# Performance work log

Hardware: AMD Instinct MI355X
Metric: run time of the kernel (lower is better)

The kernel has to match this reference:

```python
import jax, jax.numpy as jnp
import numpy as np


def _conv(x, w, pad, groups=1):
    # NCHW conv, stride 1
    return jax.lax.conv_general_dilated(
        x, w, (1, 1), [(pad, pad), (pad, pad)],
        feature_group_count=groups,
        dimension_numbers=('NCHW', 'OIHW', 'NCHW'))


def _ss2d(x, in_proj_w, conv_w, conv_b, xproj_w, dtproj_w, dtproj_b,
          A_logs, Ds, ln_g, ln_b, out_proj_w):
    # x: (B, C, H, W); VMamba-style SS2D with K=4 directional scans.
    Bb, C, H, W = x.shape
    D = conv_w.shape[0]          # d_inner = 2 * d_model
    N = A_logs.shape[-1]         # d_state
    R = dtproj_w.shape[-1]       # dt_rank
    L = H * W

    # in_proj (no bias), split into x and gate z
    xz = jnp.einsum('bchw,ec->behw', x, in_proj_w)      # (B, 2D, H, W)
    xin, z = jnp.split(xz, 2, axis=1)
    # depthwise conv + SiLU
    xc = jax.nn.silu(_conv(xin, conv_w, 1, groups=D) + conv_b[None, :, None, None])

    # build 4 scan orders: row-major, col-major, and their reverses
    xf = xc.reshape(Bb, D, L)
    xt = xc.transpose(0, 1, 3, 2).reshape(Bb, D, L)
    xs = jnp.stack([xf, xt, xf[..., ::-1], xt[..., ::-1]], axis=1)  # (B, 4, D, L)

    x_dbl = jnp.einsum('bkdl,kcd->bkcl', xs, xproj_w)   # (B, 4, R+2N, L)
    dt, Bmat, Cmat = jnp.split(x_dbl, [R, R + N], axis=2)
    delta = jax.nn.softplus(
        jnp.einsum('bkrl,kdr->bkdl', dt, dtproj_w) + dtproj_b[None, :, :, None])
    A = -jnp.exp(A_logs)                                 # (4, D, N)

    def step(h, t):
        u_t, d_t, b_t, c_t = t                           # (B,4,D),(B,4,D),(B,4,N),(B,4,N)
        h = jnp.exp(d_t[..., None] * A) * h + (d_t * u_t)[..., None] * b_t[:, :, None, :]
        return h, jnp.einsum('bkdn,bkn->bkd', h, c_t)

    tm = lambda a: jnp.moveaxis(a, -1, 0)                # time-major
    h0 = jnp.zeros((Bb, 4, D, N), x.dtype)
    _, ys = jax.lax.scan(step, h0, (tm(xs), tm(delta), tm(Bmat), tm(Cmat)))
    out_y = jnp.moveaxis(ys, 0, -1) + Ds[None, :, :, None] * xs    # (B, 4, D, L)

    inv_y = out_y[:, 2:4, :, ::-1]
    unT = lambda a: a.reshape(Bb, D, W, H).transpose(0, 1, 3, 2).reshape(Bb, D, L)
    y = out_y[:, 0] + inv_y[:, 0] + unT(out_y[:, 1]) + unT(inv_y[:, 1])  # (B, D, L)

    y = y.reshape(Bb, D, H, W).transpose(0, 2, 3, 1)     # (B, H, W, D)
    mu = y.mean(-1, keepdims=True)
    var = y.var(-1, keepdims=True)
    y = (y - mu) / jnp.sqrt(var + 1e-5) * ln_g + ln_b    # out_norm (LayerNorm)
    y = y * jax.nn.silu(z.transpose(0, 2, 3, 1))         # gate
    out = jnp.einsum('bhwd,cd->bhwc', y, out_proj_w)     # out_proj (no bias)
    return out.transpose(0, 3, 1, 2)                     # back to NCHW


def _forward(x, fc1_w, bn1_s, bn1_b, dw3_w, dw3_b, pw1_w, pw1_b,
             dw5_w, dw5_b, pw2_w, pw2_b, fc2_w, bn2_s, bn2_b,
             in_proj_w, conv_w, conv_b, xproj_w, dtproj_w, dtproj_b,
             A_logs, Ds, ln_g, ln_b, out_proj_w):
    relu6 = lambda v: jnp.clip(v, 0.0, 6.0)
    Cc = x.shape[1]
    # fc1: 1x1 conv + folded BN + ReLU6
    h = relu6(_conv(x, fc1_w, 0) * bn1_s[None, :, None, None] + bn1_b[None, :, None, None])
    Ch = h.shape[1]
    # depthwise(3) + pointwise
    x1 = _conv(_conv(h, dw3_w, 1, groups=Ch) + dw3_b[None, :, None, None], pw1_w, 0) \
         + pw1_b[None, :, None, None]
    # depthwise(5) + pointwise
    x2 = _conv(_conv(h, dw5_w, 2, groups=Ch) + dw5_b[None, :, None, None], pw2_w, 0) \
         + pw2_b[None, :, None, None]
    # SS2D attention branch
    x3 = _ss2d(h, in_proj_w, conv_w, conv_b, xproj_w, dtproj_w, dtproj_b,
               A_logs, Ds, ln_g, ln_b, out_proj_w)
    # fc2: 1x1 conv + folded BN, then ReLU6
    out = relu6(_conv(x1 + x2 + x3, fc2_w, 0) * bn2_s[None, :, None, None]
                + bn2_b[None, :, None, None])
    return out


def setup_inputs() -> dict:
    key = jax.random.key(0)
    ks = jax.random.split(key, 24)
    B, C, H, W = 4, 96, 64, 64
    D, N, R, K = 192, 16, 6, 4   # d_inner=2*96, d_state, dt_rank=ceil(96/16), 4 scans
    rn = lambda k, s, sc: jax.random.normal(k, s, jnp.float32) * sc
    return {
        'x': rn(ks[0], (B, C, H, W), 1.0),
        'fc1_w': rn(ks[1], (C, C, 1, 1), 0.1),
        'bn1_s': 1.0 + rn(ks[2], (C,), 0.05),
        'bn1_b': rn(ks[3], (C,), 0.05),
        'dw3_w': rn(ks[4], (C, 1, 3, 3), 0.2),
        'dw3_b': rn(ks[5], (C,), 0.02),
        'pw1_w': rn(ks[6], (C, C, 1, 1), 0.1),
        'pw1_b': rn(ks[7], (C,), 0.02),
        'dw5_w': rn(ks[8], (C, 1, 5, 5), 0.1),
        'dw5_b': rn(ks[9], (C,), 0.02),
        'pw2_w': rn(ks[10], (C, C, 1, 1), 0.1),
        'pw2_b': rn(ks[11], (C,), 0.02),
        'fc2_w': rn(ks[12], (C, C, 1, 1), 0.1),
        'bn2_s': 1.0 + rn(ks[13], (C,), 0.05),
        'bn2_b': rn(ks[14], (C,), 0.05),
        'in_proj_w': rn(ks[15], (2 * D, C), 0.05),
        'conv_w': rn(ks[16], (D, 1, 3, 3), 0.2),
        'conv_b': rn(ks[17], (D,), 0.02),
        'xproj_w': rn(ks[18], (K, R + 2 * N, D), 0.05),
        'dtproj_w': rn(ks[19], (K, D, R), 0.1),
        'dtproj_b': jnp.full((K, D), float(np.log(np.expm1(0.01))), jnp.float32)
                    + rn(ks[20], (K, D), 0.1),
        'A_logs': jnp.broadcast_to(
            jnp.log(jnp.arange(1, N + 1, dtype=jnp.float32)), (K, D, N)) + 0.0,
        'Ds': jnp.ones((K, D), jnp.float32),
        'ln_g': jnp.ones((D,), jnp.float32),
        'ln_b': jnp.zeros((D,), jnp.float32),
        'out_proj_w': rn(ks[21], (C, D), 0.05),
    }


def reference(x, fc1_w, bn1_s, bn1_b, dw3_w, dw3_b, pw1_w, pw1_b,
              dw5_w, dw5_b, pw2_w, pw2_b, fc2_w, bn2_s, bn2_b,
              in_proj_w, conv_w, conv_b, xproj_w, dtproj_w, dtproj_b,
              A_logs, Ds, ln_g, ln_b, out_proj_w):
    return _forward(x, fc1_w, bn1_s, bn1_b, dw3_w, dw3_b, pw1_w, pw1_b,
                    dw5_w, dw5_b, pw2_w, pw2_b, fc2_w, bn2_s, bn2_b,
                    in_proj_w, conv_w, conv_b, xproj_w, dtproj_w, dtproj_b,
                    A_logs, Ds, ln_g, ln_b, out_proj_w)
```

## Files before the change

### kernel.cpp

```cpp
#include <hip/hip_runtime.h>
#include <hip/hip_bf16.h>

typedef __hip_bfloat16 bf16;

#define HW 4096
#define LOG2E 1.44269504088896f
#define NSEG 128
#define SEGLEN 32
#define XROW 40

__device__ __forceinline__ float silu_f(float x){ return x / (1.f + exp2f(-x*LOG2E)); }
__device__ __forceinline__ float relu6_f(float v){ return v < 0.f ? 0.f : (v > 6.f ? 6.f : v); }

#define PW_STORE 0
#define PW_ACC 1
#define PW_RELU6_F32 2
#define PW_RELU6_OUT 3
#define PW_STORE_T 4

struct PtrTab { const void* p[25]; int off[26]; };

__global__ __launch_bounds__(256) void convert_kernel(PtrTab tab, const unsigned int* araw, float* dst, int total){
  int isb = (*araw != 0u);
  for (int i = blockIdx.x*256 + threadIdx.x; i < total; i += gridDim.x*256){
    int s = 0;
    while (s < 24 && i >= tab.off[s+1]) s++;
    int j = i - tab.off[s];
    dst[i] = isb ? __bfloat162float(((const bf16*)tab.p[s])[j])
                 : ((const float*)tab.p[s])[j];
  }
}

template<int CIN>
__global__ __launch_bounds__(256) void pw_kernel(
    const float* __restrict__ in, const float* __restrict__ inT,
    const void* __restrict__ rawin,
    const float* __restrict__ w,
    const float* __restrict__ sc, const float* __restrict__ bi,
    float* __restrict__ outf, void* __restrict__ outv, const unsigned int* __restrict__ flagp,
    int CS, int ci0, int wstride, int Cout, int mode, int xsmode, int kchunks)
{
  __shared__ float in_s[CIN*64];
  __shared__ float w_s[CIN*34];
  int t = threadIdx.x;
  int gb = blockIdx.x * 64;
  int b = gb >> 12;
  int l0 = gb & 4095;
  if (xsmode) w += (size_t)(b & 3) * Cout * wstride;
  int coc = blockIdx.y * 32;
  int lg = t & 15, cg = t >> 4;

  float a00=0.f,a01=0.f,a10=0.f,a11=0.f,a20=0.f,a21=0.f,a30=0.f,a31=0.f;

  for (int kc = 0; kc < kchunks; kc++){
    int cbase = ci0 + kc*CIN;
    if (xsmode){
      int k = b & 3, breal = b >> 2;
      const float* src = (k & 1) ? inT : in;
      int rev = (k >= 2);
      for (int e = t; e < CIN*64; e += 256){
        int ci = e >> 6, j = e & 63;
        int pos = rev ? (4095 - (l0 + j)) : (l0 + j);
        in_s[e] = src[(size_t)(breal*192 + cbase + ci)*HW + pos];
      }
    } else if (rawin){
      int isb = (*flagp != 0u);
      for (int e = t; e < CIN*64; e += 256){
        int ci = e >> 6, j = e & 63;
        size_t idx = (size_t)(b*CS + cbase + ci)*HW + l0 + j;
        in_s[e] = isb ? __bfloat162float(((const bf16*)rawin)[idx])
                      : ((const float*)rawin)[idx];
      }
    } else {
      for (int e = t; e < CIN*64; e += 256){
        int ci = e >> 6, j = e & 63;
        in_s[e] = in[(size_t)(b*CS + cbase + ci)*HW + l0 + j];
      }
    }
    for (int e = t; e < CIN*32; e += 256){
      int cc = e / CIN, ci = e - cc*CIN;
      int co = coc + cc;
      w_s[ci*34 + cc] = (co < Cout) ? w[(size_t)co*wstride + cbase + ci] : 0.f;
    }
    __syncthreads();

    for (int ci = 0; ci < CIN; ci++){
      float4 iv = *(const float4*)(in_s + ci*64 + 4*lg);
      float2 wv = *(const float2*)(w_s + ci*34 + 2*cg);
      a00 += iv.x*wv.x; a01 += iv.x*wv.y;
      a10 += iv.y*wv.x; a11 += iv.y*wv.y;
      a20 += iv.z*wv.x; a21 += iv.z*wv.y;
      a30 += iv.w*wv.x; a31 += iv.w*wv.y;
    }
    if (kc + 1 < kchunks) __syncthreads();
  }

  float accv[4][2] = {{a00,a01},{a10,a11},{a20,a21},{a30,a31}};
  for (int jj = 0; jj < 2; jj++){
    int co = coc + 2*cg + jj;
    if (co >= Cout) continue;
    float add = bi ? bi[co] : 0.f;
    if (mode == PW_STORE_T){
      int pos = (co < 6) ? co : co + 2;
      for (int i=0;i<4;i++){
        size_t a = ((size_t)b*HW + l0 + 4*lg + i)*XROW + pos;
        outf[a] = accv[i][jj] + add;
      }
      continue;
    }
    size_t base = (size_t)(b*Cout + co)*HW + l0 + 4*lg;
    if (mode == PW_STORE){
      for (int i=0;i<4;i++) outf[base+i] = accv[i][jj] + add;
    } else if (mode == PW_ACC){
      for (int i=0;i<4;i++) outf[base+i] += accv[i][jj] + add;
    } else if (mode == PW_RELU6_F32){
      float s = sc[co];
      for (int i=0;i<4;i++) outf[base+i] = relu6_f(accv[i][jj]*s + add);
    } else {
      float s = sc[co];
      int isb = (*flagp != 0u);
      for (int i=0;i<4;i++){
        float v = relu6_f(accv[i][jj]*s + add);
        if (isb) ((bf16*)outv)[base+i] = __float2bfloat16(v);
        else     ((float*)outv)[base+i] = v;
      }
    }
  }
}

__global__ __launch_bounds__(256) void pwdual_kernel(
    const float* __restrict__ inA, const float* __restrict__ wA, const float* __restrict__ biA,
    const float* __restrict__ inB, const float* __restrict__ wB, const float* __restrict__ biB,
    float* __restrict__ outf)
{
  __shared__ float in_s[96*64];
  __shared__ float w_s[96*34];
  int t = threadIdx.x;
  int gb = blockIdx.x * 64;
  int b = gb >> 12;
  int l0 = gb & 4095;
  int coc = blockIdx.y * 32;
  int lg = t & 15, cg = t >> 4;

  float a00=0.f,a01=0.f,a10=0.f,a11=0.f,a20=0.f,a21=0.f,a30=0.f,a31=0.f;

  for (int kc = 0; kc < 2; kc++){
    const float* in = kc ? inB : inA;
    const float* w  = kc ? wB  : wA;
    for (int e = t; e < 96*64; e += 256){
      int ci = e >> 6, j = e & 63;
      in_s[e] = in[(size_t)(b*96 + ci)*HW + l0 + j];
    }
    for (int e = t; e < 96*32; e += 256){
      int cc = e / 96, ci = e - cc*96;
      w_s[ci*34 + cc] = w[(size_t)(coc+cc)*96 + ci];
    }
    __syncthreads();
    for (int ci = 0; ci < 96; ci++){
      float4 iv = *(const float4*)(in_s + ci*64 + 4*lg);
      float2 wv = *(const float2*)(w_s + ci*34 + 2*cg);
      a00 += iv.x*wv.x; a01 += iv.x*wv.y;
      a10 += iv.y*wv.x; a11 += iv.y*wv.y;
      a20 += iv.z*wv.x; a21 += iv.z*wv.y;
      a30 += iv.w*wv.x; a31 += iv.w*wv.y;
    }
    if (kc == 0) __syncthreads();
  }

  float accv[4][2] = {{a00,a01},{a10,a11},{a20,a21},{a30,a31}};
  for (int jj = 0; jj < 2; jj++){
    int co = coc + 2*cg + jj;
    float add = biA[co] + biB[co];
    size_t base = (size_t)(b*96 + co)*HW + l0 + 4*lg;
    for (int i=0;i<4;i++) outf[base+i] = accv[i][jj] + add;
  }
}

__global__ __launch_bounds__(256) void dwb_kernel(
  const float* __restrict__ h, const float* __restrict__ w3, const float* __restrict__ b3,
  const float* __restrict__ w5, const float* __restrict__ b5,
  float* __restrict__ t3, float* __restrict__ t5)
{
  __shared__ float halo[68*68];
  int ch = blockIdx.x;
  int c = ch % 96;
  const float* src = h + (size_t)ch*HW;
  size_t off = (size_t)ch*HW;
  int t = threadIdx.x;

  for (int e = t; e < 68*68; e += 256){
    int rr = e / 68, cc = e - rr*68;
    int y = rr - 2, x = cc - 2;
    halo[e] = (y >= 0 && y < 64 && x >= 0 && x < 64) ? src[y*64 + x] : 0.f;
  }
  float wv3[9], wv5[25];
  for (int i=0;i<9;i++)  wv3[i] = w3[c*9 + i];
  for (int i=0;i<25;i++) wv5[i] = w5[c*25 + i];
  float bias3 = b3[c], bias5 = b5[c];
  __syncthreads();

  int x = t & 63, r0 = t >> 6;
  for (int s = 0; s < 16; s++){
    int y = s*4 + r0;
    float a5 = bias5;
    #pragma unroll
    for (int dy=0; dy<5; dy++)
      #pragma unroll
      for (int dx=0; dx<5; dx++)
        a5 += halo[(y+dy)*68 + (x+dx)] * wv5[dy*5+dx];
    float a3 = bias3;
    #pragma unroll
    for (int dy=0; dy<3; dy++)
      #pragma unroll
      for (int dx=0; dx<3; dx++)
        a3 += halo[(y+1+dy)*68 + (x+1+dx)] * wv3[dy*3+dx];
    t3[off + y*64 + x] = a3;
    t5[off + y*64 + x] = a5;
  }
}

__global__ __launch_bounds__(256) void dwct_kernel(
  const float* __restrict__ xz, const float* __restrict__ w, const float* __restrict__ bi,
  float* __restrict__ xc, float* __restrict__ xcT)
{
  __shared__ float halo[66*66];
  __shared__ float tileT[64*65];
  int ch = blockIdx.x;
  int b = ch / 192, c = ch % 192;
  const float* src = xz + ((size_t)(b*384) + c)*HW;
  size_t off = (size_t)ch*HW;
  int t = threadIdx.x;

  for (int e = t; e < 66*66; e += 256){
    int rr = e / 66, cc = e - rr*66;
    int y = rr - 1, x = cc - 1;
    halo[e] = (y >= 0 && y < 64 && x >= 0 && x < 64) ? src[y*64 + x] : 0.f;
  }
  float wv[9];
  for (int i=0;i<9;i++) wv[i] = w[c*9 + i];
  float bias = bi[c];
  __syncthreads();

  int c2 = t & 63, r0 = t >> 6;
  for (int s = 0; s < 16; s++){
    int r = s*4 + r0;
    float acc = bias;
    #pragma unroll
    for (int dy=0; dy<3; dy++)
      #pragma unroll
      for (int dx=0; dx<3; dx++)
        acc += halo[(r+dy)*66 + (c2+dx)] * wv[dy*3+dx];
    acc = silu_f(acc);
    xc[off + r*64 + c2] = acc;
    tileT[c2*65 + r] = acc;
  }
  __syncthreads();
  for (int s = 0; s < 16; s++){
    int r = s*4 + r0;
    xcT[off + r*64 + c2] = tileT[r*65 + c2];
  }
}

__global__ __launch_bounds__(256) void transpose_kernel(const float* __restrict__ src, const float* __restrict__ src2, float* __restrict__ dst)
{
  __shared__ float tile[64*65];
  int ch = blockIdx.x;
  size_t off = (size_t)ch*HW;
  int c = threadIdx.x & 63, r0 = threadIdx.x >> 6;
  for (int s = 0; s < 16; s++){
    int r = s*4 + r0;
    float v = src[off + r*64 + c];
    if (src2) v += src2[off + r*64 + c];
    tile[c*65 + r] = v;
  }
  __syncthreads();
  for (int s = 0; s < 16; s++){
    int r = s*4 + r0;
    dst[off + r*64 + c] = tile[r*65 + c];
  }
}

template<int PASS>
__global__ __launch_bounds__(192) void scan_kernel(
  const float* __restrict__ xc, const float* __restrict__ xcT,
  const float* __restrict__ xdblT,
  const float* __restrict__ dtw, const float* __restrict__ dtb,
  const float* __restrict__ Ds,
  float* __restrict__ Pbuf, float* __restrict__ qbuf,
  const float* __restrict__ hinit,
  float* __restrict__ oy0, float* __restrict__ oy1T,
  float* __restrict__ oy2, float* __restrict__ oy3T)
{
  __shared__ float u_s[192*17];
  __shared__ float y_s[(PASS==2) ? 16*193 : 1];

  int d = threadIdx.x;
  int s = blockIdx.x, k = blockIdx.y, b = blockIdx.z;
  int bk = b*4 + k;
  const float* usrc = (k & 1) ? xcT : xc;
  int rev = (k >= 2);

  float w6[7];
  for (int r=0;r<6;r++) w6[r] = dtw[(size_t)(k*192+d)*6 + r];
  w6[6] = dtb[k*192 + d];
  float Dv = Ds[k*192 + d];

  float st[16];
  float sdv = 0.f;
  size_t pqbase = ((size_t)(bk*NSEG + s)*192 + d)*16;
  if (PASS==1){
    for (int n=0;n<16;n++) st[n]=0.f;
  } else {
    const float4* hp = (const float4*)(hinit + pqbase);
    float4 h0=hp[0], h1=hp[1], h2=hp[2], h3=hp[3];
    st[0]=h0.x; st[1]=h0.y; st[2]=h0.z; st[3]=h0.w;
    st[4]=h1.x; st[5]=h1.y; st[6]=h1.z; st[7]=h1.w;
    st[8]=h2.x; st[9]=h2.y; st[10]=h2.z; st[11]=h2.w;
    st[12]=h3.x; st[13]=h3.y; st[14]=h3.z; st[15]=h3.w;
  }

  const float* rowbase = xdblT + (size_t)bk*HW*XROW;

  for (int c = 0; c < SEGLEN/16; c++){
    int l0c = s*SEGLEN + c*16;
    for (int e = d; e < 192*16; e += 192){
      int j = e & 15, d2 = e >> 4;
      int pos = rev ? (4095 - (l0c + j)) : (l0c + j);
      u_s[d2*17+j] = usrc[((size_t)(b*192 + d2))*HW + pos];
    }
    __syncthreads();

    const float* rp = rowbase + (size_t)l0c*XROW;
    #pragma unroll
    for (int j=0;j<16;j++){
      float4 dt03 = *(const float4*)(rp);
      float2 dt45 = *(const float2*)(rp + 4);
      float v = w6[6] + dt03.x*w6[0] + dt03.y*w6[1] + dt03.z*w6[2] + dt03.w*w6[3]
                      + dt45.x*w6[4] + dt45.y*w6[5];
      float t = exp2f(v*LOG2E);
      float rr = 1.f/(1.f + t);
      float dv = (v > 20.f) ? v : log2f(1.f + t)*(1.f/LOG2E);
      float uv = u_s[d*17+j];
      float du = dv*uv;
      float4 B0 = *(const float4*)(rp + 8);
      float4 B1 = *(const float4*)(rp + 12);
      float4 B2 = *(const float4*)(rp + 16);
      float4 B3 = *(const float4*)(rp + 20);
      float Bv[16] = {B0.x,B0.y,B0.z,B0.w, B1.x,B1.y,B1.z,B1.w,
                      B2.x,B2.y,B2.z,B2.w, B3.x,B3.y,B3.z,B3.w};
      float a = rr;
      if (PASS==1){
        sdv += dv;
        #pragma unroll
        for (int n=0;n<16;n++){
          st[n] = a*st[n] + du*Bv[n];
          a *= rr;
        }
      } else {
        float4 C0 = *(const float4*)(rp + 24);
        float4 C1 = *(const float4*)(rp + 28);
        float4 C2 = *(const float4*)(rp + 32);
        float4 C3 = *(const float4*)(rp + 36);
        float Cv[16] = {C0.x,C0.y,C0.z,C0.w, C1.x,C1.y,C1.z,C1.w,
                        C2.x,C2.y,C2.z,C2.w, C3.x,C3.y,C3.z,C3.w};
        float y = Dv*uv;
        #pragma unroll
        for (int n=0;n<16;n++){
          st[n] = a*st[n] + du*Bv[n];
          y += st[n]*Cv[n];
          a *= rr;
        }
        y_s[j*193 + d] = y;
      }
      rp += XROW;
    }
    __syncthreads();
    if (PASS==2){
      float* dst = (k==0) ? oy0 : (k==1) ? oy1T : (k==2) ? oy2 : oy3T;
      for (int e = d; e < 16*192; e += 192){
        int j = e & 15, d2 = e >> 4;
        int pos = rev ? (4095 - (l0c + j)) : (l0c + j);
        dst[((size_t)(b*192 + d2))*HW + pos] = y_s[j*193 + d2];
      }
    }
  }

  if (PASS==1){
    float rT = exp2f(-sdv*LOG2E);
    float Pv[16];
    float pw = rT;
    for (int n=0;n<16;n++){ Pv[n]=pw; pw*=rT; }
    float4* Pp = (float4*)(Pbuf + pqbase);
    float4* qp = (float4*)(qbuf + pqbase);
    for (int i=0;i<4;i++){
      Pp[i] = make_float4(Pv[4*i], Pv[4*i+1], Pv[4*i+2], Pv[4*i+3]);
      qp[i] = make_float4(st[4*i], st[4*i+1], st[4*i+2], st[4*i+3]);
    }
  }
}

__global__ __launch_bounds__(256) void stitch_kernel(const float* __restrict__ P, float* __restrict__ q)
{
  int gid = blockIdx.x*256 + threadIdx.x;
  int n = gid & 15;
  int rest = gid >> 4;
  int d = rest % 192;
  int bk = rest / 192;
  float h = 0.f;
  for (int s = 0; s < NSEG; s++){
    size_t idx = (((size_t)bk*NSEG + s)*192 + d)*16 + n;
    float Pv = P[idx];
    float qv = q[idx];
    q[idx] = h;
    h = Pv*h + qv;
  }
}

__global__ __launch_bounds__(256) void combineproj_kernel(
  const float* __restrict__ oy0, const float* __restrict__ oy2, const float* __restrict__ oyTt,
  const float* __restrict__ xz, const float* __restrict__ ln_g, const float* __restrict__ ln_b,
  const float* __restrict__ opw, float* __restrict__ accb)
{
  __shared__ float ysh[192*36];
  __shared__ float ws[192*33];
  __shared__ float ps[8*32];
  __shared__ float pq[8*32];
  __shared__ float mu_s[32];
  __shared__ float rs_s[32];
  int t = threadIdx.x;
  int l0 = blockIdx.x*32, b = blockIdx.y;
  int c = t & 31, r0 = t >> 5;

  for (int i = 0; i < 24; i++){
    int r = i*8 + r0;
    size_t idx = ((size_t)(b*192 + r))*HW + l0 + c;
    ysh[r*36 + c] = oy0[idx] + oy2[idx] + oyTt[idx];
  }
  __syncthreads();
  {
    float s1 = 0.f, s2 = 0.f;
    for (int i = 0; i < 24; i++){
      int r = r0*24 + i;
      float v = ysh[r*36 + c];
      s1 += v; s2 += v*v;
    }
    ps[r0*32 + c] = s1; pq[r0*32 + c] = s2;
  }
  __syncthreads();
  if (t < 32){
    float s1 = 0.f, s2 = 0.f;
    for (int g = 0; g < 8; g++){ s1 += ps[g*32 + t]; s2 += pq[g*32 + t]; }
    float mu = s1 * (1.f/192.f);
    float var = s2 * (1.f/192.f) - mu*mu;
    mu_s[t] = mu;
    rs_s[t] = rsqrtf(var + 1e-5f);
  }
  __syncthreads();
  for (int i = 0; i < 24; i++){
    int r = i*8 + r0;
    float v = (ysh[r*36+c] - mu_s[c]) * rs_s[c] * ln_g[r] + ln_b[r];
    float zv = xz[((size_t)(b*384 + 192 + r))*HW + l0 + c];
    ysh[r*36+c] = v * silu_f(zv);
  }

  int lg = t & 7, cg = t >> 3;
  for (int cochunk = 0; cochunk < 3; cochunk++){
    int coc = cochunk*32;
    __syncthreads();
    for (int e = t; e < 32*192; e += 256){
      int cc = e / 192, ci = e - cc*192;
      ws[ci*33 + cc] = opw[(size_t)(coc+cc)*192 + ci];
    }
    __syncthreads();
    float a0=0.f,a1=0.f,a2=0.f,a3=0.f;
    for (int ci = 0; ci < 192; ci++){
      float4 yv = *(const float4*)(ysh + ci*36 + 4*lg);
      float wv = ws[ci*33 + cg];
      a0 += yv.x*wv; a1 += yv.y*wv; a2 += yv.z*wv; a3 += yv.w*wv;
    }
    int co = coc + cg;
    size_t base = ((size_t)(b*96 + co))*HW + l0 + 4*lg;
    accb[base+0] += a0; accb[base+1] += a1; accb[base+2] += a2; accb[base+3] += a3;
  }
}

extern "C" void kernel_launch(void* const* d_in, const int* in_sizes, int n_in,
                              void* d_out, int out_size, void* d_ws, size_t ws_size,
                              hipStream_t stream)
{
  float* ws = (float*)d_ws;
  size_t off = 0;
  auto alloc = [&](size_t n){ float* p = ws + off; off += n; return p; };

  const unsigned int* araw = (const unsigned int*)d_in[21];

  PtrTab tab;
  tab.off[0] = 0;
  for (int i = 0; i < 25; i++){
    tab.p[i] = d_in[i+1];
    tab.off[i+1] = tab.off[i] + in_sizes[i+1];
  }
  int total = tab.off[25];
  float* conv_base = alloc((size_t)total);
  const float* fc1_w  = conv_base + tab.off[0];
  const float* bn1_s  = conv_base + tab.off[1];
  const float* bn1_b  = conv_base + tab.off[2];
  const float* dw3_w  = conv_base + tab.off[3];
  const float* dw3_b  = conv_base + tab.off[4];
  const float* pw1_w  = conv_base + tab.off[5];
  const float* pw1_b  = conv_base + tab.off[6];
  const float* dw5_w  = conv_base + tab.off[7];
  const float* dw5_b  = conv_base + tab.off[8];
  const float* pw2_w  = conv_base + tab.off[9];
  const float* pw2_b  = conv_base + tab.off[10];
  const float* fc2_w  = conv_base + tab.off[11];
  const float* bn2_s  = conv_base + tab.off[12];
  const float* bn2_b  = conv_base + tab.off[13];
  const float* inp_w  = conv_base + tab.off[14];
  const float* convw  = conv_base + tab.off[15];
  const float* convb  = conv_base + tab.off[16];
  const float* xprojw = conv_base + tab.off[17];
  const float* dtw    = conv_base + tab.off[18];
  const float* dtb    = conv_base + tab.off[19];
  const float* dsv    = conv_base + tab.off[21];
  const float* lng    = conv_base + tab.off[22];
  const float* lnb    = conv_base + tab.off[23];
  const float* outpw  = conv_base + tab.off[24];

  float* hbuf   = alloc(1572864);
  float* tbuf   = alloc(1572864);
  float* accb   = alloc(1572864);
  float* xz     = alloc(6291456);
  float* xc     = alloc(3145728);
  float* xcT    = alloc(3145728);
  float* xdblT  = alloc(2621440);
  float* Pb     = alloc(6291456);
  float* qb     = alloc(6291456);
  float* oy1T   = alloc(3145728);
  float* oy3T   = alloc(3145728);
  float* oyTt   = alloc(3145728);
  float* oy0    = hbuf;
  float* oy2    = Pb;
  float* t5     = oy1T;

  convert_kernel<<<(total+255)/256,256,0,stream>>>(tab, araw, conv_base, total);
  pw_kernel<96><<<dim3(256,3),256,0,stream>>>(nullptr, nullptr, d_in[0], fc1_w, bn1_s, bn1_b, hbuf, nullptr, araw, 96,0,96, 96, PW_RELU6_F32, 0, 1);
  pw_kernel<96><<<dim3(256,12),256,0,stream>>>(hbuf, nullptr, nullptr, inp_w, nullptr, nullptr, xz, nullptr, nullptr, 96,0,96, 384, PW_STORE, 0, 1);
  dwb_kernel<<<384,256,0,stream>>>(hbuf, dw3_w, dw3_b, dw5_w, dw5_b, tbuf, t5);
  pwdual_kernel<<<dim3(256,3),256,0,stream>>>(tbuf, pw1_w, pw1_b, t5, pw2_w, pw2_b, accb);
  dwct_kernel<<<768,256,0,stream>>>(xz, convw, convb, xc, xcT);
  pw_kernel<96><<<dim3(1024,2),256,0,stream>>>(xc, xcT, nullptr, xprojw, nullptr, nullptr, xdblT, nullptr, nullptr, 192,0,192, 38, PW_STORE_T, 1, 2);
  scan_kernel<1><<<dim3(NSEG,4,4),192,0,stream>>>(xc, xcT, xdblT, dtw, dtb, dsv, Pb, qb, nullptr, nullptr, nullptr, nullptr, nullptr);
  stitch_kernel<<<192,256,0,stream>>>(Pb, qb);
  scan_kernel<2><<<dim3(NSEG,4,4),192,0,stream>>>(xc, xcT, xdblT, dtw, dtb, dsv, nullptr, nullptr, qb, oy0, oy1T, oy2, oy3T);
  transpose_kernel<<<768,256,0,stream>>>(oy1T, oy3T, oyTt);
  combineproj_kernel<<<dim3(128,4),256,0,stream>>>(oy0, oy2, oyTt, xz, lng, lnb, outpw, accb);
  pw_kernel<96><<<dim3(256,3),256,0,stream>>>(accb, nullptr, nullptr, fc2_w, bn2_s, bn2_b, nullptr, d_out, araw, 96,0,96, 96, PW_RELU6_OUT, 0, 1);

  (void)n_in; (void)ws_size; (void)out_size;
}
```

Before: 454.3 us.

## Run pointwise projections on bf16 MFMA instead of fp32 FMA loops

```diff
diff --git a/kernel.cpp b/kernel.cpp
--- a/kernel.cpp
+++ b/kernel.cpp
@@ -11,12 +11,19 @@
 
 __device__ __forceinline__ float silu_f(float x){ return x / (1.f + exp2f(-x*LOG2E)); }
 __device__ __forceinline__ float relu6_f(float v){ return v < 0.f ? 0.f : (v > 6.f ? 6.f : v); }
+__device__ __forceinline__ unsigned short f2bs(float f){
+  bf16 h = __float2bfloat16(f);
+  return *(unsigned short*)&h;
+}
 
 #define PW_STORE 0
 #define PW_ACC 1
 #define PW_RELU6_F32 2
 #define PW_RELU6_OUT 3
 #define PW_STORE_T 4
+
+using frag_ab = __attribute__((ext_vector_type(8))) short;
+using frag_cd = __attribute__((ext_vector_type(4))) float;
 
 struct PtrTab { const void* p[25]; int off[26]; };
 
@@ -28,6 +35,111 @@
     int j = i - tab.off[s];
     dst[i] = isb ? __bfloat162float(((const bf16*)tab.p[s])[j])
                  : ((const float*)tab.p[s])[j];
+  }
+}
+
+__global__ __launch_bounds__(256) void cvtw_kernel(
+  const float* s0, unsigned short* d0p, int n0,
+  const float* s1, unsigned short* d1p, int n1,
+  const float* s2, unsigned short* d2p, int n2)
+{
+  int total = n0+n1+n2;
+  for (int i = blockIdx.x*256+threadIdx.x; i < total; i += gridDim.x*256){
+    if (i < n0) d0p[i] = f2bs(s0[i]);
+    else if (i < n0+n1) d1p[i-n0] = f2bs(s1[i-n0]);
+    else d2p[i-n0-n1] = f2bs(s2[i-n0-n1]);
+  }
+}
+
+__global__ __launch_bounds__(256) void pwmfma_kernel(
+    const float* __restrict__ in, const float* __restrict__ inT,
+    const void* __restrict__ rawin,
+    const unsigned short* __restrict__ wb,
+    const float* __restrict__ sc, const float* __restrict__ bi,
+    float* __restrict__ outf, const unsigned int* __restrict__ flagp,
+    int CS, int Kfull, int Cout, int mode, int xsmode, int kchunks)
+{
+  __shared__ __align__(16) unsigned short in_sT[64*104];
+  int t = threadIdx.x;
+  int gb = blockIdx.x * 64;
+  int b = gb >> 12;
+  int l0 = gb & 4095;
+  int coc = blockIdx.y * 32;
+  const unsigned short* wbase = wb;
+  if (xsmode) wbase += (size_t)(b & 3) * Cout * Kfull;
+
+  int lane = t & 63, wv = t >> 6;
+  int n = lane & 15, q = lane >> 4;
+  int lrow = 16*wv + n;
+
+  frag_cd d0 = {0.f,0.f,0.f,0.f}, d1 = {0.f,0.f,0.f,0.f};
+  int co0c = min(coc + n, Cout-1);
+  int co1c = min(coc + 16 + n, Cout-1);
+
+  for (int kc_ = 0; kc_ < kchunks; kc_++){
+    int cbase = kc_*96;
+    if (xsmode){
+      int k = b & 3, breal = b >> 2;
+      const float* src = (k & 1) ? inT : in;
+      int rev = (k >= 2);
+      for (int e = t; e < 96*64; e += 256){
+        int ci = e >> 6, j = e & 63;
+        int pos = rev ? (4095 - (l0 + j)) : (l0 + j);
+        in_sT[j*104 + ci] = f2bs(src[(size_t)(breal*192 + cbase + ci)*HW + pos]);
+      }
+    } else if (rawin){
+      int isb = (*flagp != 0u);
+      if (isb){
+        const unsigned short* rs = (const unsigned short*)rawin;
+        for (int e = t; e < 96*64; e += 256){
+          int ci = e >> 6, j = e & 63;
+          in_sT[j*104 + ci] = rs[(size_t)(b*CS + cbase + ci)*HW + l0 + j];
+        }
+      } else {
+        const float* rf = (const float*)rawin;
+        for (int e = t; e < 96*64; e += 256){
+          int ci = e >> 6, j = e & 63;
+          in_sT[j*104 + ci] = f2bs(rf[(size_t)(b*CS + cbase + ci)*HW + l0 + j]);
+        }
+      }
+    } else {
+      for (int e = t; e < 96*64; e += 256){
+        int ci = e >> 6, j = e & 63;
+        in_sT[j*104 + ci] = f2bs(in[(size_t)(b*CS + cbase + ci)*HW + l0 + j]);
+      }
+    }
+    __syncthreads();
+
+    #pragma unroll
+    for (int kc = 0; kc < 96; kc += 32){
+      int kk = cbase + kc + q*8;
+      frag_ab a0 = *(const frag_ab*)(wbase + (size_t)co0c*Kfull + kk);
+      frag_ab a1 = *(const frag_ab*)(wbase + (size_t)co1c*Kfull + kk);
+      frag_ab bf = *(const frag_ab*)(in_sT + lrow*104 + kc + q*8);
+      d0 = __builtin_amdgcn_mfma_f32_16x16x32_bf16(a0, bf, d0, 0, 0, 0);
+      d1 = __builtin_amdgcn_mfma_f32_16x16x32_bf16(a1, bf, d1, 0, 0, 0);
+    }
+    if (kc_ + 1 < kchunks) __syncthreads();
+  }
+
+  int lidx = l0 + lrow;
+  #pragma unroll
+  for (int h = 0; h < 2; h++){
+    frag_cd dd = h ? d1 : d0;
+    #pragma unroll
+    for (int r = 0; r < 4; r++){
+      int co = coc + 16*h + 4*q + r;
+      if (co >= Cout) continue;
+      float v = dd[r];
+      if (mode == PW_RELU6_F32) v = relu6_f(v*sc[co] + bi[co]);
+      else if (bi) v += bi[co];
+      if (mode == PW_STORE_T){
+        int pos = (co < 6) ? co : co + 2;
+        outf[((size_t)b*HW + lidx)*XROW + pos] = v;
+      } else {
+        outf[(size_t)(b*Cout + co)*HW + lidx] = v;
+      }
+    }
   }
 }
 
@@ -54,16 +166,7 @@
 
   for (int kc = 0; kc < kchunks; kc++){
     int cbase = ci0 + kc*CIN;
-    if (xsmode){
-      int k = b & 3, breal = b >> 2;
-      const float* src = (k & 1) ? inT : in;
-      int rev = (k >= 2);
-      for (int e = t; e < CIN*64; e += 256){
-        int ci = e >> 6, j = e & 63;
-        int pos = rev ? (4095 - (l0 + j)) : (l0 + j);
-        in_s[e] = src[(size_t)(breal*192 + cbase + ci)*HW + pos];
-      }
-    } else if (rawin){
+    if (rawin){
       int isb = (*flagp != 0u);
       for (int e = t; e < CIN*64; e += 256){
         int ci = e >> 6, j = e & 63;
@@ -100,14 +203,6 @@
     int co = coc + 2*cg + jj;
     if (co >= Cout) continue;
     float add = bi ? bi[co] : 0.f;
-    if (mode == PW_STORE_T){
-      int pos = (co < 6) ? co : co + 2;
-      for (int i=0;i<4;i++){
-        size_t a = ((size_t)b*HW + l0 + 4*lg + i)*XROW + pos;
-        outf[a] = accv[i][jj] + add;
-      }
-      continue;
-    }
     size_t base = (size_t)(b*Cout + co)*HW + l0 + 4*lg;
     if (mode == PW_STORE){
       for (int i=0;i<4;i++) outf[base+i] = accv[i][jj] + add;
@@ -490,7 +585,7 @@
 {
   float* ws = (float*)d_ws;
   size_t off = 0;
-  auto alloc = [&](size_t n){ float* p = ws + off; off += n; return p; };
+  auto alloc = [&](size_t n){ float* p = ws + off; off += (n + 3) & ~(size_t)3; return p; };
 
   const unsigned int* araw = (const unsigned int*)d_in[21];
 
@@ -527,6 +622,10 @@
   const float* lnb    = conv_base + tab.off[23];
   const float* outpw  = conv_base + tab.off[24];
 
+  unsigned short* fc1wb = (unsigned short*)alloc(9216/2 + 4);
+  unsigned short* inpwb = (unsigned short*)alloc(36864/2 + 4);
+  unsigned short* xprwb = (unsigned short*)alloc(29184/2 + 4);
+
   float* hbuf   = alloc(1572864);
   float* tbuf   = alloc(1572864);
   float* accb   = alloc(1572864);
@@ -544,18 +643,19 @@
   float* t5     = oy1T;
 
   convert_kernel<<<(total+255)/256,256,0,stream>>>(tab, araw, conv_base, total);
-  pw_kernel<96><<<dim3(256,3),256,0,stream>>>(nullptr, nullptr, d_in[0], fc1_w, bn1_s, bn1_b, hbuf, nullptr, araw, 96,0,96, 96, PW_RELU6_F32, 0, 1);
-  pw_kernel<96><<<dim3(256,12),256,0,stream>>>(hbuf, nullptr, nullptr, inp_w, nullptr, nullptr, xz, nullptr, nullptr, 96,0,96, 384, PW_STORE, 0, 1);
+  cvtw_kernel<<<295,256,0,stream>>>(fc1_w, fc1wb, 9216, inp_w, inpwb, 36864, xprojw, xprwb, 29184);
+  pwmfma_kernel<<<dim3(256,3),256,0,stream>>>(nullptr, nullptr, d_in[0], fc1wb, bn1_s, bn1_b, hbuf, araw, 96, 96, 96, PW_RELU6_F32, 0, 1);
+  pwmfma_kernel<<<dim3(256,12),256,0,stream>>>(hbuf, nullptr, nullptr, inpwb, nullptr, nullptr, xz, nullptr, 96, 96, 384, PW_STORE, 0, 1);
   dwb_kernel<<<384,256,0,stream>>>(hbuf, dw3_w, dw3_b, dw5_w, dw5_b, tbuf, t5);
   pwdual_kernel<<<dim3(256,3),256,0,stream>>>(tbuf, pw1_w, pw1_b, t5, pw2_w, pw2_b, accb);
   dwct_kernel<<<768,256,0,stream>>>(xz, convw, convb, xc, xcT);
-  pw_kernel<96><<<dim3(1024,2),256,0,stream>>>(xc, xcT, nullptr, xprojw, nullptr, nullptr, xdblT, nullptr, nullptr, 192,0,192, 38, PW_STORE_T, 1, 2);
+  pwmfma_kernel<<<dim3(1024,2),256,0,stream>>>(xc, xcT, nullptr, xprwb, nullptr, nullptr, xdblT, nullptr, 192, 192, 38, PW_STORE_T, 1, 2);
   scan_kernel<1><<<dim3(NSEG,4,4),192,0,stream>>>(xc, xcT, xdblT, dtw, dtb, dsv, Pb, qb, nullptr, nullptr, nullptr, nullptr, nullptr);
   stitch_kernel<<<192,256,0,stream>>>(Pb, qb);
   scan_kernel<2><<<dim3(NSEG,4,4),192,0,stream>>>(xc, xcT, xdblT, dtw, dtb, dsv, nullptr, nullptr, qb, oy0, oy1T, oy2, oy3T);
   transpose_kernel<<<768,256,0,stream>>>(oy1T, oy3T, oyTt);
   combineproj_kernel<<<dim3(128,4),256,0,stream>>>(oy0, oy2, oyTt, xz, lng, lnb, outpw, accb);
-  pw_kernel<96><<<dim3(256,3),256,0,stream>>>(accb, nullptr, nullptr, fc2_w, bn2_s, bn2_b, nullptr, d_out, araw, 96,0,96, 96, PW_RELU6_OUT, 0, 1);
+  pw_kernel<96><<<dim3(256,3),256,0,stream>>>(accb, nullptr, nullptr, fc2_w, bn2_s, bn2_b, nullptr, d_out, araw, 96, 0, 96, 96, PW_RELU6_OUT, 0, 1);
 
   (void)n_in; (void)ws_size; (void)out_size;
 }
```

Result: faster. 444.5 us (-2.2%).
